# Kernel optimization log

Hardware: AMD Instinct MI355X
Metric: run time of the kernel (lower is better)

## Reference

```python
import jax, jax.numpy as jnp
import numpy as np
import math

D_MODEL = 1024
N_HEADS = 16
D_K = D_MODEL // N_HEADS
D_FF = 4096
B = 2
S = 2048
LN_EPS = 1e-3  # Keras LayerNormalization default


def setup_inputs() -> dict:
    key = jax.random.key(0)
    ks = jax.random.split(key, 16)
    s = 0.02
    inp = {
        "x": jax.random.normal(ks[0], (B, S, D_MODEL), dtype=jnp.float32),
        "weights": jax.random.uniform(ks[1], (B, S), dtype=jnp.float32),
        # attention projections (Dense: y = x @ W + b)
        "Wq": jax.random.normal(ks[2], (D_MODEL, D_MODEL), jnp.float32) * s,
        "bq": jnp.zeros((D_MODEL,), jnp.float32),
        "Wk": jax.random.normal(ks[3], (D_MODEL, D_MODEL), jnp.float32) * s,
        "bk": jnp.zeros((D_MODEL,), jnp.float32),
        "Wv": jax.random.normal(ks[4], (D_MODEL, D_MODEL), jnp.float32) * s,
        "bv": jnp.zeros((D_MODEL,), jnp.float32),
        "Wo": jax.random.normal(ks[5], (D_MODEL, D_MODEL), jnp.float32) * s,
        "bo": jnp.zeros((D_MODEL,), jnp.float32),
        # FFN
        "W1": jax.random.normal(ks[6], (D_MODEL, D_FF), jnp.float32) * s,
        "b1": jnp.zeros((D_FF,), jnp.float32),
        "W2": jax.random.normal(ks[7], (D_FF, D_MODEL), jnp.float32) * s,
        "b2": jnp.zeros((D_MODEL,), jnp.float32),
        # layer norms
        "g1": jnp.ones((D_MODEL,), jnp.float32),
        "be1": jnp.zeros((D_MODEL,), jnp.float32),
        "g2": jnp.ones((D_MODEL,), jnp.float32),
        "be2": jnp.zeros((D_MODEL,), jnp.float32),
    }
    return inp


def _layer_norm(x, gamma, beta):
    mu = jnp.mean(x, axis=-1, keepdims=True)
    var = jnp.mean(jnp.square(x - mu), axis=-1, keepdims=True)
    return (x - mu) * jax.lax.rsqrt(var + LN_EPS) * gamma + beta


def _block(x, weights, Wq, bq, Wk, bk, Wv, bv, Wo, bo, W1, b1, W2, b2, g1, be1, g2, be2):
    b, s, _ = x.shape
    # projections -> (B, H, S, d_k)
    def split_heads(y):
        return y.reshape(b, s, N_HEADS, D_K).transpose(0, 2, 1, 3)
    Q = split_heads(x @ Wq + bq)
    K = split_heads(x @ Wk + bk)
    V = split_heads(x @ Wv + bv)
    scores = jnp.einsum("bhqd,bhkd->bhqk", Q, K) / math.sqrt(D_K)
    log_w = jnp.log(weights + 1e-20)[:, None, None, :]  # (B,1,1,S)
    attn = jax.nn.softmax(scores + log_w, axis=-1)
    out = jnp.einsum("bhqk,bhkd->bhqd", attn, V)
    out = out.transpose(0, 2, 1, 3).reshape(b, s, D_MODEL)
    attn_out = out @ Wo + bo
    h = _layer_norm(x + attn_out, g1, be1)
    ffn = jax.nn.relu(h @ W1 + b1) @ W2 + b2
    return _layer_norm(h + ffn, g2, be2)


def reference(x, weights, Wq, bq, Wk, bk, Wv, bv, Wo, bo, W1, b1, W2, b2, g1, be1, g2, be2):
    return _block(x, weights, Wq, bq, Wk, bk, Wv, bv, Wo, bo, W1, b1, W2, b2, g1, be1, g2, be2)
```

## Files before the change

### kernel.cpp

```cpp
#include <hip/hip_runtime.h>
#include <cstdint>
#include <cstddef>

#define DM 1024
#define NH 16
#define DKH 64
#define DFF 4096
#define NB 2
#define SQL 2048
#define MROWS (NB * SQL)
#define QKVN 3072

typedef __attribute__((ext_vector_type(8))) __bf16 bf16x8;
typedef __attribute__((ext_vector_type(8))) short short8;
typedef __attribute__((ext_vector_type(4))) float f32x4;

__device__ __forceinline__ unsigned short f2bf(float f) {
    unsigned u = __float_as_uint(f);
    u += 0x7fffu + ((u >> 16) & 1u);
    return (unsigned short)(u >> 16);
}
__device__ __forceinline__ bf16x8 ldfrag(const unsigned short* p) {
    return __builtin_bit_cast(bf16x8, *(const short8*)p);
}
__device__ __forceinline__ void gl_lds16(const void* g, void* lds) {
    __builtin_amdgcn_global_load_lds(
        (const __attribute__((address_space(1))) unsigned int*)g,
        (__attribute__((address_space(3))) unsigned int*)lds, 16, 0, 0);
}
#define MFMA16(a, b, c) __builtin_amdgcn_mfma_f32_16x16x32_bf16(a, b, c, 0, 0, 0)

#define QSCALE 0.18033688011112042f

__global__ __launch_bounds__(256) void prep_all(const float* __restrict__ Wq,
                                                const float* __restrict__ Wk,
                                                const float* __restrict__ Wv,
                                                const float* __restrict__ Wo,
                                                const float* __restrict__ W1,
                                                const float* __restrict__ W2,
                                                const float* __restrict__ x,
                                                const float* __restrict__ wts,
                                                const float* __restrict__ bq,
                                                const float* __restrict__ bk,
                                                const float* __restrict__ bv,
                                                unsigned short* __restrict__ wqkv_t,
                                                unsigned short* __restrict__ Wo_t,
                                                unsigned short* __restrict__ W1_t,
                                                unsigned short* __restrict__ W2_t,
                                                unsigned short* __restrict__ x_bf,
                                                float* __restrict__ logw,
                                                float* __restrict__ bqkv) {
    const int t = blockIdx.x, tid = threadIdx.x;
    if (t >= 12288) {
        if (t < 16384) {
            int i = ((t - 12288) * 256 + tid) * 4;
            float4 v = *(const float4*)&x[i];
            ushort4 o;
            o.x = f2bf(v.x); o.y = f2bf(v.y); o.z = f2bf(v.z); o.w = f2bf(v.w);
            *(ushort4*)&x_bf[i] = o;
        } else if (t < 16400) {
            int i = (t - 16384) * 256 + tid;
            logw[i] = log2f(wts[i] + 1e-20f);
        } else {
            int i = (t - 16400) * 256 + tid;
            if (i < QKVN)
                bqkv[i] = i < 1024 ? bq[i] * QSCALE : (i < 2048 ? bk[i - 1024] : bv[i - 2048]);
        }
        return;
    }
    __shared__ float tile[32][33];
    const float* in;
    unsigned short* out;
    int K = DM, N = DM, n0, k0;
    float scale = 1.f;
    if (t < 1024)      { in = Wq; out = wqkv_t;                      scale = QSCALE;
                         n0 = (t & 31) * 32;          k0 = (t >> 5) * 32; }
    else if (t < 2048) { in = Wk; out = wqkv_t + (size_t)1024 * DM;
                         n0 = ((t - 1024) & 31) * 32; k0 = ((t - 1024) >> 5) * 32; }
    else if (t < 3072) { in = Wv; out = wqkv_t + (size_t)2048 * DM;
                         n0 = ((t - 2048) & 31) * 32; k0 = ((t - 2048) >> 5) * 32; }
    else if (t < 4096) { in = Wo; out = Wo_t;
                         n0 = ((t - 3072) & 31) * 32; k0 = ((t - 3072) >> 5) * 32; }
    else if (t < 8192) { in = W1; out = W1_t; N = DFF;
                         n0 = ((t - 4096) & 127) * 32; k0 = ((t - 4096) >> 7) * 32; }
    else               { in = W2; out = W2_t; K = DFF;
                         n0 = ((t - 8192) & 31) * 32;  k0 = ((t - 8192) >> 5) * 32; }
    const int tx = threadIdx.x & 31, ty = threadIdx.x >> 5;
#pragma unroll
    for (int i = 0; i < 32; i += 8)
        tile[ty + i][tx] = in[(size_t)(k0 + ty + i) * N + n0 + tx];
    __syncthreads();
#pragma unroll
    for (int i = 0; i < 32; i += 8)
        out[(size_t)(n0 + ty + i) * K + k0 + tx] = f2bf(tile[tx][ty + i] * scale);
}

template <int BN, bool RELU, int OMODE, int KSPL>
__global__ __launch_bounds__(256) void gemm_kernel(const unsigned short* __restrict__ A,
                                                   const unsigned short* __restrict__ Wt,
                                                   const float* __restrict__ bias,
                                                   void* __restrict__ outp,
                                                   unsigned short* __restrict__ vtp,
                                                   int M, int N, int K) {
    constexpr int NT = BN / 32;
    __shared__ unsigned short As[128 * 64];
    __shared__ unsigned short Bs[BN * 64];
    const int tid = threadIdx.x;
    const int wave = tid >> 6, lane = tid & 63;
    const int col16 = lane & 15, quad = lane >> 4;
    const int lrow = lane >> 3, sblk = (lane & 7) ^ (lrow & 7);
    const int f = blockIdx.y * gridDim.x + blockIdx.x;
    const int nper = gridDim.x >> 3;
    const int bx = (f & 7) * nper + (f >> 3) % nper;
    const int by = (f >> 3) / nper;
    const int m0 = by * 128, n0 = bx * BN;
    const int wm = (wave >> 1) * 64, wn = (wave & 1) * (BN / 2);
    const int kbeg = (KSPL > 1) ? blockIdx.z * (K / KSPL) : 0;
    const int kend = kbeg + K / KSPL;

    f32x4 acc[4][NT] = {};

    for (int k0 = kbeg; k0 < kend; k0 += 64) {
        __syncthreads();
#pragma unroll
        for (int c = wave; c < 16; c += 4)
            gl_lds16(&A[(size_t)(m0 + c * 8 + lrow) * K + k0 + sblk * 8], &As[c * 512]);
#pragma unroll
        for (int c = wave; c < BN / 8; c += 4)
            gl_lds16(&Wt[(size_t)(n0 + c * 8 + lrow) * K + k0 + sblk * 8], &Bs[c * 512]);
        __syncthreads();
#pragma unroll
        for (int kk8 = 0; kk8 < 8; kk8 += 4) {
            bf16x8 af[4], bfr[NT];
#pragma unroll
            for (int t = 0; t < 4; ++t) {
                int R = wm + t * 16 + col16;
                af[t] = ldfrag(&As[R * 64 + (((kk8 + quad) ^ (R & 7)) << 3)]);
            }
#pragma unroll
            for (int t = 0; t < NT; ++t) {
                int R = wn + t * 16 + col16;
                bfr[t] = ldfrag(&Bs[R * 64 + (((kk8 + quad) ^ (R & 7)) << 3)]);
            }
#pragma unroll
            for (int mt = 0; mt < 4; ++mt)
#pragma unroll
                for (int nt = 0; nt < NT; ++nt)
                    acc[mt][nt] = MFMA16(af[mt], bfr[nt], acc[mt][nt]);
        }
    }

    float* outf = (float*)outp + ((KSPL > 1) ? (size_t)blockIdx.z * M * N : 0);
#pragma unroll
    for (int mt = 0; mt < 4; ++mt)
#pragma unroll
        for (int nt = 0; nt < NT; ++nt) {
            int col = n0 + wn + nt * 16 + col16;
            float bv = (KSPL == 1 || blockIdx.z == 0) ? bias[col] : 0.f;
            if (OMODE == 2 && col >= 2048) {
                int dl = (col - 2048) & 63, hh = (col - 2048) >> 6;
                int row0 = m0 + wm + mt * 16 + quad * 4;
                int bb = row0 >> 11, sb = row0 & 2047;
                ushort4 w4;
                w4.x = f2bf(acc[mt][nt][0] + bv);
                w4.y = f2bf(acc[mt][nt][1] + bv);
                w4.z = f2bf(acc[mt][nt][2] + bv);
                w4.w = f2bf(acc[mt][nt][3] + bv);
                *(ushort4*)&vtp[(size_t)(bb * NH + hh) * DKH * SQL + (size_t)dl * SQL + sb] = w4;
            } else {
#pragma unroll
                for (int r = 0; r < 4; ++r) {
                    int row = m0 + wm + mt * 16 + quad * 4 + r;
                    float v = acc[mt][nt][r] + bv;
                    if (RELU) v = fmaxf(v, 0.f);
                    if (OMODE == 0)
                        outf[(size_t)row * N + col] = v;
                    else
                        ((unsigned short*)outp)[(size_t)row * N + col] = f2bf(v);
                }
            }
        }
}

template <int OMODE, bool RELU>
__global__ __launch_bounds__(512, 2) void gemm256_kernel(const unsigned short* __restrict__ A,
                                                         const unsigned short* __restrict__ Wt,
                                                         const float* __restrict__ bias,
                                                         void* __restrict__ outp,
                                                         unsigned short* __restrict__ vtp,
                                                         int M, int N, int K) {
    __shared__ __align__(16) unsigned short Ab[2][2][256 * 32];
    __shared__ __align__(16) unsigned short Bb[2][2][256 * 32];
    const int tid = threadIdx.x, wave = tid >> 6, lane = tid & 63;
    const int col16 = lane & 15, quad = lane >> 4;
    const int f = blockIdx.y * gridDim.x + blockIdx.x;
    const int nwg = gridDim.x * gridDim.y, q8 = nwg >> 3;
    const int wg = (f & 7) * q8 + (f >> 3);
    const int bx = wg % gridDim.x, by = wg / gridDim.x;
    const int m0 = by * 256, n0 = bx * 256;
    const int wm = (wave >> 2) * 128, wn = (wave & 3) * 64;
    const int rS = wave * 32 + (lane >> 2);
    const int cS = ((lane & 3) ^ (rS & 3)) << 3;
    const unsigned short* srcA = A + (size_t)(m0 + rS) * K + cS;
    const unsigned short* srcB = Wt + (size_t)(n0 + rS) * K + cS;
    const int NTt = K >> 6, NI = NTt >> 1;

    f32x4 acc[8][4] = {};
    bf16x8 af[4], bfr[4];

#define STGA(t, kh) { int ts = (t) < NTt ? (t) : NTt - 1;                          \
    const unsigned short* s_ = srcA + (((size_t)ts) << 6) + ((kh) << 5);           \
    unsigned short* d_ = &Ab[(t) & 1][kh][wave * 1024];                            \
    gl_lds16(s_, d_); gl_lds16(s_ + (size_t)16 * K, d_ + 512); }
#define STGB(t, kh) { int ts = (t) < NTt ? (t) : NTt - 1;                          \
    const unsigned short* s_ = srcB + (((size_t)ts) << 6) + ((kh) << 5);           \
    unsigned short* d_ = &Bb[(t) & 1][kh][wave * 1024];                            \
    gl_lds16(s_, d_); gl_lds16(s_ + (size_t)16 * K, d_ + 512); }
#define LDA(mf, buf, kh) ({ int R_ = wm + (mf) * 16 + col16;                       \
    ldfrag(&Ab[buf][kh][R_ * 32 + ((quad ^ (R_ & 3)) << 3)]); })
#define LDB(nf, buf, kh) ({ int R_ = wn + (nf) * 16 + col16;                       \
    ldfrag(&Bb[buf][kh][R_ * 32 + ((quad ^ (R_ & 3)) << 3)]); })
#define PHASE_EVEN(buf, kh) {                                                      \
    asm volatile("s_waitcnt vmcnt(10)" ::: "memory");                              \
    __builtin_amdgcn_s_barrier();                                                  \
    bfr[0] = LDB(0, buf, kh); bfr[1] = LDB(1, buf, kh);                            \
    bfr[2] = LDB(2, buf, kh); bfr[3] = LDB(3, buf, kh);                            \
    af[0] = LDA(0, buf, kh); af[1] = LDA(1, buf, kh);                              \
    af[2] = LDA(2, buf, kh); af[3] = LDA(3, buf, kh);                              \
    __builtin_amdgcn_s_setprio(1);                                                 \
    _Pragma("unroll") for (int mt = 0; mt < 4; ++mt)                               \
        _Pragma("unroll") for (int nt = 0; nt < 4; ++nt)                           \
            acc[mt][nt] = MFMA16(af[mt], bfr[nt], acc[mt][nt]);                    \
    __builtin_amdgcn_s_setprio(0);                                                 \
    __builtin_amdgcn_s_barrier(); }
#define PHASE_ODD(buf, kh) {                                                       \
    __builtin_amdgcn_s_barrier();                                                  \
    af[0] = LDA(4, buf, kh); af[1] = LDA(5, buf, kh);                              \
    af[2] = LDA(6, buf, kh); af[3] = LDA(7, buf, kh);                              \
    __builtin_amdgcn_s_setprio(1);                                                 \
    _Pragma("unroll") for (int mt = 0; mt < 4; ++mt)                               \
        _Pragma("unroll") for (int nt = 0; nt < 4; ++nt)                           \
            acc[4 + mt][nt] = MFMA16(af[mt], bfr[nt], acc[4 + mt][nt]);            \
    __builtin_amdgcn_s_setprio(0);                                                 \
    __builtin_amdgcn_s_barrier(); }

    STGA(0, 0); STGB(0, 0);
    STGA(0, 1); STGB(0, 1);
    STGA(1, 0); STGB(1, 0);

    for (int i = 0; i < NI; ++i) {
        const int t2 = i * 2;
        STGA(t2 + 1, 1); PHASE_EVEN(0, 0);
        STGB(t2 + 1, 1); PHASE_ODD(0, 0);
        STGA(t2 + 2, 0); PHASE_EVEN(0, 1);
        STGB(t2 + 2, 0); PHASE_ODD(0, 1);
        STGA(t2 + 2, 1); PHASE_EVEN(1, 0);
        STGB(t2 + 2, 1); PHASE_ODD(1, 0);
        STGA(t2 + 3, 0); PHASE_EVEN(1, 1);
        STGB(t2 + 3, 0); PHASE_ODD(1, 1);
    }
#undef STGA
#undef STGB
#undef LDA
#undef LDB
#undef PHASE_EVEN
#undef PHASE_ODD

#pragma unroll
    for (int mf = 0; mf < 8; ++mf)
#pragma unroll
        for (int nf = 0; nf < 4; ++nf) {
            int col = n0 + wn + nf * 16 + col16;
            float bv = bias[col];
            if (OMODE == 2 && col >= 2048) {
                int dl = (col - 2048) & 63, hh = (col - 2048) >> 6;
                int row0 = m0 + wm + mf * 16 + quad * 4;
                int bb = row0 >> 11, sb = row0 & 2047;
                ushort4 w4;
                w4.x = f2bf(acc[mf][nf][0] + bv);
                w4.y = f2bf(acc[mf][nf][1] + bv);
                w4.z = f2bf(acc[mf][nf][2] + bv);
                w4.w = f2bf(acc[mf][nf][3] + bv);
                *(ushort4*)&vtp[(size_t)(bb * NH + hh) * DKH * SQL + (size_t)dl * SQL + sb] = w4;
            } else {
#pragma unroll
                for (int r = 0; r < 4; ++r) {
                    int row = m0 + wm + mf * 16 + quad * 4 + r;
                    float v = acc[mf][nf][r] + bv;
                    if (RELU) v = fmaxf(v, 0.f);
                    ((unsigned short*)outp)[(size_t)row * N + col] = f2bf(v);
                }
            }
        }
}

__global__ __launch_bounds__(512) void flash_kernel(const unsigned short* __restrict__ qkv,
                                                    const unsigned short* __restrict__ vt,
                                                    const float* __restrict__ logw,
                                                    unsigned short* __restrict__ attn_bf) {
    __shared__ unsigned short Ks[2][64 * 64];
    __shared__ unsigned short Vt[2][64 * 64];
    __shared__ unsigned short Ps[8][16][72];
    __shared__ float lws[2][64];

    const int tid = threadIdx.x, wave = tid >> 6, lane = tid & 63;
    const int col16 = lane & 15, quad = lane >> 4;
    const int lrow = lane >> 3, sblk = (lane & 7) ^ (lrow & 7);
    const int f = blockIdx.y * gridDim.x + blockIdx.x;
    const int g = f >> 3;
    const int bh = (f & 7) * 4 + (g & 3);
    const int q0 = (g >> 2) * 128;
    const int b = bh >> 4, h = bh & 15;

    const unsigned short* Kg = qkv + (size_t)b * SQL * QKVN + 1024 + h * DKH;
    const unsigned short* Vg = vt + (size_t)bh * DKH * SQL;

    bf16x8 qf[2];
    {
        const unsigned short* qrow =
            qkv + (size_t)(b * SQL + q0 + wave * 16 + col16) * QKVN + h * DKH;
        qf[0] = ldfrag(qrow + quad * 8);
        qf[1] = ldfrag(qrow + 32 + quad * 8);
    }
    bf16x8 ones;
    {
        short8 o8 = {0x3f80, 0x3f80, 0x3f80, 0x3f80, 0x3f80, 0x3f80, 0x3f80, 0x3f80};
        ones = __builtin_bit_cast(bf16x8, o8);
    }

    f32x4 o[4] = {};
    f32x4 lacc = {};

    {
        const int c = wave;
        gl_lds16(&Kg[(size_t)(c * 8 + lrow) * QKVN + sblk * 8], &Ks[0][c * 512]);
        gl_lds16(&Vg[(size_t)(c * 8 + lrow) * SQL + sblk * 8], &Vt[0][c * 512]);
        if (tid < 64) lws[0][tid] = logw[b * SQL + tid];
    }

    int cur = 0;
    for (int kt = 0; kt < SQL; kt += 64) {
        __syncthreads();
        if (kt + 64 < SQL) {
            const int c = wave;
            gl_lds16(&Kg[(size_t)(kt + 64 + c * 8 + lrow) * QKVN + sblk * 8],
                     &Ks[cur ^ 1][c * 512]);
            gl_lds16(&Vg[(size_t)(c * 8 + lrow) * SQL + kt + 64 + sblk * 8],
                     &Vt[cur ^ 1][c * 512]);
            if (tid < 64) lws[cur ^ 1][tid] = logw[b * SQL + kt + 64 + tid];
        }

        float pv[4][4];
        __builtin_amdgcn_s_setprio(1);
#pragma unroll
        for (int nt = 0; nt < 4; ++nt) {
            int R = nt * 16 + col16;
            f32x4 s4 = {};
            s4 = MFMA16(qf[0], ldfrag(&Ks[cur][R * 64 + ((quad ^ (R & 7)) << 3)]), s4);
            s4 = MFMA16(qf[1], ldfrag(&Ks[cur][R * 64 + (((4 + quad) ^ (R & 7)) << 3)]), s4);
            float lw = lws[cur][R];
#pragma unroll
            for (int r = 0; r < 4; ++r)
                pv[nt][r] = __builtin_amdgcn_exp2f(s4[r] + lw);
        }
        __builtin_amdgcn_s_setprio(0);
#pragma unroll
        for (int nt = 0; nt < 4; ++nt)
#pragma unroll
            for (int r = 0; r < 4; ++r)
                *(__bf16*)&Ps[wave][quad * 4 + r][nt * 16 + col16] = (__bf16)pv[nt][r];

#pragma unroll
        for (int kk8 = 0; kk8 < 8; kk8 += 4) {
            bf16x8 psf = ldfrag(&Ps[wave][col16][(kk8 + quad) << 3]);
            __builtin_amdgcn_s_setprio(1);
            lacc = MFMA16(ones, psf, lacc);
#pragma unroll
            for (int dt = 0; dt < 4; ++dt) {
                int R = dt * 16 + col16;
                bf16x8 vf = ldfrag(&Vt[cur][R * 64 + (((kk8 + quad) ^ (R & 7)) << 3)]);
                o[dt] = MFMA16(vf, psf, o[dt]);
            }
            __builtin_amdgcn_s_setprio(0);
        }
        cur ^= 1;
    }

    const float rl = 1.0f / lacc[0];
    const int qrow = b * SQL + q0 + wave * 16 + col16;
#pragma unroll
    for (int dt = 0; dt < 4; ++dt) {
        ushort4 h4;
        h4.x = f2bf(o[dt][0] * rl);
        h4.y = f2bf(o[dt][1] * rl);
        h4.z = f2bf(o[dt][2] * rl);
        h4.w = f2bf(o[dt][3] * rl);
        *(ushort4*)&attn_bf[(size_t)qrow * DM + h * DKH + dt * 16 + quad * 4] = h4;
    }
}

__global__ __launch_bounds__(256) void ln1_kernel(const float* __restrict__ x,
                                                  const float* __restrict__ d0,
                                                  const float* __restrict__ d1,
                                                  const float* __restrict__ g,
                                                  const float* __restrict__ be,
                                                  float* __restrict__ hf,
                                                  unsigned short* __restrict__ hb) {
    const int row = blockIdx.x, tid = threadIdx.x;
    float4 xv = *(const float4*)&x[(size_t)row * DM + tid * 4];
    float4 av = *(const float4*)&d0[(size_t)row * DM + tid * 4];
    float4 bv = *(const float4*)&d1[(size_t)row * DM + tid * 4];
    float v[4] = {xv.x + av.x + bv.x, xv.y + av.y + bv.y, xv.z + av.z + bv.z,
                  xv.w + av.w + bv.w};
    float s = v[0] + v[1] + v[2] + v[3];
    float ss = v[0] * v[0] + v[1] * v[1] + v[2] * v[2] + v[3] * v[3];
#pragma unroll
    for (int m = 1; m < 64; m <<= 1) { s += __shfl_xor(s, m); ss += __shfl_xor(ss, m); }
    __shared__ float sb[4], ssb[4];
    if ((tid & 63) == 0) { sb[tid >> 6] = s; ssb[tid >> 6] = ss; }
    __syncthreads();
    s = sb[0] + sb[1] + sb[2] + sb[3];
    ss = ssb[0] + ssb[1] + ssb[2] + ssb[3];
    float mu = s * (1.f / DM);
    float var = fmaxf(ss * (1.f / DM) - mu * mu, 0.f);
    float rs = rsqrtf(var + 1e-3f);
#pragma unroll
    for (int i = 0; i < 4; ++i) {
        int c = tid * 4 + i;
        float y = (v[i] - mu) * rs * g[c] + be[c];
        hf[(size_t)row * DM + c] = y;
        hb[(size_t)row * DM + c] = f2bf(y);
    }
}

__global__ __launch_bounds__(256) void ln2_kernel(const float* __restrict__ hf,
                                                  const float* __restrict__ d0,
                                                  const float* __restrict__ d1,
                                                  const float* __restrict__ g,
                                                  const float* __restrict__ be,
                                                  float* __restrict__ outp) {
    const int row = blockIdx.x, tid = threadIdx.x;
    float4 hv = *(const float4*)&hf[(size_t)row * DM + tid * 4];
    float4 av = *(const float4*)&d0[(size_t)row * DM + tid * 4];
    float4 bv = *(const float4*)&d1[(size_t)row * DM + tid * 4];
    float v[4] = {hv.x + av.x + bv.x, hv.y + av.y + bv.y, hv.z + av.z + bv.z,
                  hv.w + av.w + bv.w};
    float s = v[0] + v[1] + v[2] + v[3];
    float ss = v[0] * v[0] + v[1] * v[1] + v[2] * v[2] + v[3] * v[3];
#pragma unroll
    for (int m = 1; m < 64; m <<= 1) { s += __shfl_xor(s, m); ss += __shfl_xor(ss, m); }
    __shared__ float sb[4], ssb[4];
    if ((tid & 63) == 0) { sb[tid >> 6] = s; ssb[tid >> 6] = ss; }
    __syncthreads();
    s = sb[0] + sb[1] + sb[2] + sb[3];
    ss = ssb[0] + ssb[1] + ssb[2] + ssb[3];
    float mu = s * (1.f / DM);
    float var = fmaxf(ss * (1.f / DM) - mu * mu, 0.f);
    float rs = rsqrtf(var + 1e-3f);
    float4 ov;
    ov.x = (v[0] - mu) * rs * g[tid * 4 + 0] + be[tid * 4 + 0];
    ov.y = (v[1] - mu) * rs * g[tid * 4 + 1] + be[tid * 4 + 1];
    ov.z = (v[2] - mu) * rs * g[tid * 4 + 2] + be[tid * 4 + 2];
    ov.w = (v[3] - mu) * rs * g[tid * 4 + 3] + be[tid * 4 + 3];
    *(float4*)&outp[(size_t)row * DM + tid * 4] = ov;
}

extern "C" void kernel_launch(void* const* d_in, const int* in_sizes, int n_in,
                              void* d_out, int out_size, void* d_ws, size_t ws_size,
                              hipStream_t stream) {
    const float* x   = (const float*)d_in[0];
    const float* wts = (const float*)d_in[1];
    const float* Wq  = (const float*)d_in[2];
    const float* bq  = (const float*)d_in[3];
    const float* Wk  = (const float*)d_in[4];
    const float* bk  = (const float*)d_in[5];
    const float* Wv  = (const float*)d_in[6];
    const float* bv  = (const float*)d_in[7];
    const float* Wo  = (const float*)d_in[8];
    const float* bo  = (const float*)d_in[9];
    const float* W1  = (const float*)d_in[10];
    const float* b1  = (const float*)d_in[11];
    const float* W2  = (const float*)d_in[12];
    const float* b2  = (const float*)d_in[13];
    const float* g1  = (const float*)d_in[14];
    const float* be1 = (const float*)d_in[15];
    const float* g2  = (const float*)d_in[16];
    const float* be2 = (const float*)d_in[17];

    char* ws = (char*)d_ws;
    const size_t MB = 1u << 20;
    unsigned short* qkv_bf  = (unsigned short*)(ws + 0 * MB);
    unsigned short* vt      = (unsigned short*)(ws + 24 * MB);
    unsigned short* x_bf    = (unsigned short*)(ws + 32 * MB);
    unsigned short* wqkv_t  = (unsigned short*)(ws + 40 * MB);
    unsigned short* Wo_t    = (unsigned short*)(ws + 46 * MB);
    unsigned short* W1_t    = (unsigned short*)(ws + 48 * MB);
    float* h_f32            = (float*)(ws + 64 * MB);
    unsigned short* h_bf    = (unsigned short*)(ws + 80 * MB);
    unsigned short* W2_t    = (unsigned short*)(ws + 88 * MB);
    float* bqkv             = (float*)(ws + 96 * MB);
    float* logw             = (float*)(ws + 96 * MB + 0x8000);
    unsigned short* attn_bf = (unsigned short*)(ws + 32 * MB);
    float* attnproj         = (float*)(ws + 0 * MB);
    unsigned short* ffn1_bf = (unsigned short*)(ws + 0 * MB);
    float* ffn2             = (float*)(ws + 32 * MB);

    prep_all<<<16412, 256, 0, stream>>>(Wq, Wk, Wv, Wo, W1, W2, x, wts, bq, bk, bv,
                                        wqkv_t, Wo_t, W1_t, W2_t, x_bf, logw, bqkv);

    gemm256_kernel<2, false><<<dim3(QKVN / 256, MROWS / 256), 512, 0, stream>>>(
        x_bf, wqkv_t, bqkv, qkv_bf, vt, MROWS, QKVN, DM);

    flash_kernel<<<dim3(SQL / 128, NB * NH), 512, 0, stream>>>(qkv_bf, vt, logw, attn_bf);

    gemm_kernel<64, false, 0, 2><<<dim3(DM / 64, MROWS / 128, 2), 256, 0, stream>>>(
        attn_bf, Wo_t, bo, attnproj, nullptr, MROWS, DM, DM);
    ln1_kernel<<<MROWS, 256, 0, stream>>>(x, attnproj, attnproj + (size_t)MROWS * DM,
                                          g1, be1, h_f32, h_bf);

    gemm256_kernel<1, true><<<dim3(DFF / 256, MROWS / 256), 512, 0, stream>>>(
        h_bf, W1_t, b1, ffn1_bf, nullptr, MROWS, DFF, DM);
    gemm_kernel<64, false, 0, 2><<<dim3(DM / 64, MROWS / 128, 2), 256, 0, stream>>>(
        ffn1_bf, W2_t, b2, ffn2, nullptr, MROWS, DM, DFF);
    ln2_kernel<<<MROWS, 256, 0, stream>>>(h_f32, ffn2, ffn2 + (size_t)MROWS * DM,
                                          g2, be2, (float*)d_out);
}
```

Before: 357.0 us.

## Restructure 256x256 GEMM main loop with per-tile double buffering and new LDS swizzle

Rewrites the gemm256 main loop. The old 8-phase unrolled schedule over two K-tiles becomes a single loop per 64-wide K tile that prefetches the next tile into the other buffer. Global-to-LDS staging now has each wave load 16 rows at offsets wave*16 and +128, and the LDS XOR swizzle changes to use row>>1, which aims to cut bank conflicts. It also drops some barriers and relaxes the vmcnt waits. The cost is shallower prefetch depth (one tile ahead instead of more), so memory latency may be less well hidden.

```diff
diff --git a/kernel.cpp b/kernel.cpp
--- a/kernel.cpp
+++ b/kernel.cpp
@@ -199,72 +199,87 @@
     const int bx = wg % gridDim.x, by = wg / gridDim.x;
     const int m0 = by * 256, n0 = bx * 256;
     const int wm = (wave >> 2) * 128, wn = (wave & 3) * 64;
-    const int rS = wave * 32 + (lane >> 2);
-    const int cS = ((lane & 3) ^ (rS & 3)) << 3;
-    const unsigned short* srcA = A + (size_t)(m0 + rS) * K + cS;
-    const unsigned short* srcB = Wt + (size_t)(n0 + rS) * K + cS;
-    const int NTt = K >> 6, NI = NTt >> 1;
+    const int sRow = lane >> 2;
+    const int sCol = (((lane & 3) ^ ((lane >> 3) & 3)) << 3);
+    const unsigned short* srcA = A + (size_t)(m0 + wave * 16 + sRow) * K + sCol;
+    const unsigned short* srcB = Wt + (size_t)(n0 + wave * 16 + sRow) * K + sCol;
+    const int NTt = K >> 6;
 
     f32x4 acc[8][4] = {};
     bf16x8 af[4], bfr[4];
 
-#define STGA(t, kh) { int ts = (t) < NTt ? (t) : NTt - 1;                          \
-    const unsigned short* s_ = srcA + (((size_t)ts) << 6) + ((kh) << 5);           \
-    unsigned short* d_ = &Ab[(t) & 1][kh][wave * 1024];                            \
-    gl_lds16(s_, d_); gl_lds16(s_ + (size_t)16 * K, d_ + 512); }
-#define STGB(t, kh) { int ts = (t) < NTt ? (t) : NTt - 1;                          \
-    const unsigned short* s_ = srcB + (((size_t)ts) << 6) + ((kh) << 5);           \
-    unsigned short* d_ = &Bb[(t) & 1][kh][wave * 1024];                            \
-    gl_lds16(s_, d_); gl_lds16(s_ + (size_t)16 * K, d_ + 512); }
-#define LDA(mf, buf, kh) ({ int R_ = wm + (mf) * 16 + col16;                       \
-    ldfrag(&Ab[buf][kh][R_ * 32 + ((quad ^ (R_ & 3)) << 3)]); })
-#define LDB(nf, buf, kh) ({ int R_ = wn + (nf) * 16 + col16;                       \
-    ldfrag(&Bb[buf][kh][R_ * 32 + ((quad ^ (R_ & 3)) << 3)]); })
-#define PHASE_EVEN(buf, kh) {                                                      \
-    asm volatile("s_waitcnt vmcnt(10)" ::: "memory");                              \
-    __builtin_amdgcn_s_barrier();                                                  \
-    bfr[0] = LDB(0, buf, kh); bfr[1] = LDB(1, buf, kh);                            \
-    bfr[2] = LDB(2, buf, kh); bfr[3] = LDB(3, buf, kh);                            \
-    af[0] = LDA(0, buf, kh); af[1] = LDA(1, buf, kh);                              \
-    af[2] = LDA(2, buf, kh); af[3] = LDA(3, buf, kh);                              \
-    __builtin_amdgcn_s_setprio(1);                                                 \
-    _Pragma("unroll") for (int mt = 0; mt < 4; ++mt)                               \
-        _Pragma("unroll") for (int nt = 0; nt < 4; ++nt)                           \
-            acc[mt][nt] = MFMA16(af[mt], bfr[nt], acc[mt][nt]);                    \
-    __builtin_amdgcn_s_setprio(0);                                                 \
-    __builtin_amdgcn_s_barrier(); }
-#define PHASE_ODD(buf, kh) {                                                       \
-    __builtin_amdgcn_s_barrier();                                                  \
-    af[0] = LDA(4, buf, kh); af[1] = LDA(5, buf, kh);                              \
-    af[2] = LDA(6, buf, kh); af[3] = LDA(7, buf, kh);                              \
-    __builtin_amdgcn_s_setprio(1);                                                 \
-    _Pragma("unroll") for (int mt = 0; mt < 4; ++mt)                               \
-        _Pragma("unroll") for (int nt = 0; nt < 4; ++nt)                           \
-            acc[4 + mt][nt] = MFMA16(af[mt], bfr[nt], acc[4 + mt][nt]);            \
-    __builtin_amdgcn_s_setprio(0);                                                 \
-    __builtin_amdgcn_s_barrier(); }
-
-    STGA(0, 0); STGB(0, 0);
-    STGA(0, 1); STGB(0, 1);
-    STGA(1, 0); STGB(1, 0);
-
-    for (int i = 0; i < NI; ++i) {
-        const int t2 = i * 2;
-        STGA(t2 + 1, 1); PHASE_EVEN(0, 0);
-        STGB(t2 + 1, 1); PHASE_ODD(0, 0);
-        STGA(t2 + 2, 0); PHASE_EVEN(0, 1);
-        STGB(t2 + 2, 0); PHASE_ODD(0, 1);
-        STGA(t2 + 2, 1); PHASE_EVEN(1, 0);
-        STGB(t2 + 2, 1); PHASE_ODD(1, 0);
-        STGA(t2 + 3, 0); PHASE_EVEN(1, 1);
-        STGB(t2 + 3, 0); PHASE_ODD(1, 1);
+#define STGA(ts, kh, par) { int tc = (ts) < NTt ? (ts) : NTt - 1;                 \
+    const unsigned short* s_ = srcA + (((size_t)tc) << 6) + ((kh) << 5);          \
+    gl_lds16(s_, &Ab[par][kh][wave * 512]);                                       \
+    gl_lds16(s_ + (size_t)128 * K, &Ab[par][kh][(wave + 8) * 512]); }
+#define STGB(ts, kh, par) { int tc = (ts) < NTt ? (ts) : NTt - 1;                 \
+    const unsigned short* s_ = srcB + (((size_t)tc) << 6) + ((kh) << 5);          \
+    gl_lds16(s_, &Bb[par][kh][wave * 512]);                                       \
+    gl_lds16(s_ + (size_t)128 * K, &Bb[par][kh][(wave + 8) * 512]); }
+#define LDA(mf, par, kh) ({ int R_ = wm + (mf) * 16 + col16;                      \
+    ldfrag(&Ab[par][kh][R_ * 32 + (((quad ^ (R_ >> 1)) & 3) << 3)]); })
+#define LDB(nf, par, kh) ({ int R_ = wn + (nf) * 16 + col16;                      \
+    ldfrag(&Bb[par][kh][R_ * 32 + (((quad ^ (R_ >> 1)) & 3) << 3)]); })
+
+    STGB(0, 0, 0); STGA(0, 0, 0); STGB(0, 1, 0); STGA(0, 1, 0);
+
+    for (int t = 0; t < NTt; ++t) {
+        const int par = t & 1, pn = par ^ 1, t1 = t + 1;
+        STGB(t1, 0, pn);
+        asm volatile("s_waitcnt vmcnt(6)" ::: "memory");
+        __builtin_amdgcn_s_barrier();
+        bfr[0] = LDB(0, par, 0); bfr[1] = LDB(1, par, 0);
+        bfr[2] = LDB(2, par, 0); bfr[3] = LDB(3, par, 0);
+        af[0] = LDA(0, par, 0); af[1] = LDA(1, par, 0);
+        af[2] = LDA(2, par, 0); af[3] = LDA(3, par, 0);
+        __builtin_amdgcn_s_setprio(1);
+#pragma unroll
+        for (int mt = 0; mt < 4; ++mt)
+#pragma unroll
+            for (int nt = 0; nt < 4; ++nt)
+                acc[mt][nt] = MFMA16(af[mt], bfr[nt], acc[mt][nt]);
+        __builtin_amdgcn_s_setprio(0);
+        __builtin_amdgcn_s_barrier();
+        af[0] = LDA(4, par, 0); af[1] = LDA(5, par, 0);
+        af[2] = LDA(6, par, 0); af[3] = LDA(7, par, 0);
+        STGA(t1, 0, pn);
+        __builtin_amdgcn_s_setprio(1);
+#pragma unroll
+        for (int mt = 0; mt < 4; ++mt)
+#pragma unroll
+            for (int nt = 0; nt < 4; ++nt)
+                acc[4 + mt][nt] = MFMA16(af[mt], bfr[nt], acc[4 + mt][nt]);
+        __builtin_amdgcn_s_setprio(0);
+        STGB(t1, 1, pn);
+        asm volatile("s_waitcnt vmcnt(6)" ::: "memory");
+        __builtin_amdgcn_s_barrier();
+        bfr[0] = LDB(0, par, 1); bfr[1] = LDB(1, par, 1);
+        bfr[2] = LDB(2, par, 1); bfr[3] = LDB(3, par, 1);
+        af[0] = LDA(0, par, 1); af[1] = LDA(1, par, 1);
+        af[2] = LDA(2, par, 1); af[3] = LDA(3, par, 1);
+        __builtin_amdgcn_s_setprio(1);
+#pragma unroll
+        for (int mt = 0; mt < 4; ++mt)
+#pragma unroll
+            for (int nt = 0; nt < 4; ++nt)
+                acc[mt][nt] = MFMA16(af[mt], bfr[nt], acc[mt][nt]);
+        __builtin_amdgcn_s_setprio(0);
+        __builtin_amdgcn_s_barrier();
+        af[0] = LDA(4, par, 1); af[1] = LDA(5, par, 1);
+        af[2] = LDA(6, par, 1); af[3] = LDA(7, par, 1);
+        STGA(t1, 1, pn);
+        __builtin_amdgcn_s_setprio(1);
+#pragma unroll
+        for (int mt = 0; mt < 4; ++mt)
+#pragma unroll
+            for (int nt = 0; nt < 4; ++nt)
+                acc[4 + mt][nt] = MFMA16(af[mt], bfr[nt], acc[4 + mt][nt]);
+        __builtin_amdgcn_s_setprio(0);
     }
 #undef STGA
 #undef STGB
 #undef LDA
 #undef LDB
-#undef PHASE_EVEN
-#undef PHASE_ODD
 
 #pragma unroll
     for (int mf = 0; mf < 8; ++mf)
```

Result: faster. 347.7 us (-2.6%).
